# Performance work log

Measured on AMD Instinct MI355X. Metric: run time of the kernel, lower is better.

Reference implementation:

```python
import jax, jax.numpy as jnp
import numpy as np

B, H, W, C = 32, 56, 56, 256
WS = 7            # window size (hard-coded 49=7*7 in original topk modules)
NH = 8            # num heads
HD = C // NH      # head dim = 32
KCH = HD // 2     # channel top-k = 16
KSPT = 28         # spatial top-k
N = WS * WS       # 49 tokens per window
SCALE = HD ** -0.5
MLP_H = 4 * C

def _rel_index(ws):
    coords = np.stack(np.meshgrid(np.arange(ws), np.arange(ws), indexing='ij')).reshape(2, -1)
    rc = (coords[:, :, None] - coords[:, None, :]).transpose(1, 2, 0).astype(np.int64)
    rc[:, :, 0] += ws - 1
    rc[:, :, 1] += ws - 1
    rc[:, :, 0] *= 2 * ws - 1
    return jnp.asarray(rc.sum(-1))  # (N, N)

REL_IDX = _rel_index(WS)

def setup_inputs():
    key = jax.random.key(0)
    ks = jax.random.split(key, 10)
    p = lambda k, shp: jax.random.normal(k, shp, jnp.float32) * 0.02
    return dict(
        x=jax.random.normal(ks[0], (B, H * W, C), jnp.float32),
        norm1_g=jnp.ones((C,), jnp.float32), norm1_b=jnp.zeros((C,), jnp.float32),
        wq=p(ks[1], (C, C)), bq=jnp.zeros((C,), jnp.float32),
        wk=p(ks[2], (C // 2, C // 2)), bk=jnp.zeros((C // 2,), jnp.float32),
        wv=p(ks[3], (C, C)), bv=jnp.zeros((C,), jnp.float32),
        wproj=p(ks[4], (C, C)), bproj=jnp.zeros((C,), jnp.float32),
        wch=p(ks[5], (2 * HD, HD)), bch=jnp.zeros((HD,), jnp.float32),
        rpb_table=p(ks[6], ((2 * WS - 1) ** 2, NH)),
        norm2_g=jnp.ones((C,), jnp.float32), norm2_b=jnp.zeros((C,), jnp.float32),
        w1=p(ks[7], (C, MLP_H)), b1=jnp.zeros((MLP_H,), jnp.float32),
        w2=p(ks[8], (MLP_H, C)), b2=jnp.zeros((C,), jnp.float32),
    )

def _ln(x, g, b):
    mu = x.mean(-1, keepdims=True)
    var = x.var(-1, keepdims=True)
    return (x - mu) / jnp.sqrt(var + 1e-5) * g + b

def reference(x, norm1_g, norm1_b, wq, bq, wk, bk, wv, bv, wproj, bproj,
              wch, bch, rpb_table, norm2_g, norm2_b, w1, b1, w2, b2):
    shortcut = x
    xn = _ln(x, norm1_g, norm1_b).reshape(B, H, W, C)
    # window partition -> (Bw, N, C)
    xw = xn.reshape(B, H // WS, WS, W // WS, WS, C).transpose(0, 1, 3, 2, 4, 5).reshape(-1, N, C)
    Bw = xw.shape[0]
    q = xw @ wq + bq                                                    # (Bw, N, C)
    qh = q.reshape(Bw, N, NH, HD).transpose(0, 2, 1, 3).reshape(Bw * NH, N, HD)
    # ---- channel top-k (ChannelTopk) ----
    feat = jnp.concatenate([qh.mean(1), qh.max(1)], axis=-1)            # (Bn, 2*HD)
    score = jax.nn.softmax(jax.nn.gelu(feat @ wch + bch, approximate=False), axis=1)
    _, cidx = jax.lax.top_k(score, KCH)
    cidx = jnp.sort(cidx, axis=-1)                                      # sorted channel indices
    qcha = jnp.take_along_axis(qh, cidx[:, None, :], axis=2)            # (Bn, N, KCH)
    qcha1 = qcha.reshape(Bw, NH, N, KCH).transpose(0, 2, 1, 3).reshape(Bw, N, C // 2)
    k = qcha1 @ wk + bk                                                 # (Bw, N, C/2)
    # ---- relative position bias ----
    rpb = rpb_table[REL_IDX.reshape(-1)].reshape(N, N, NH).transpose(2, 0, 1)  # (NH, N, N)
    # ---- spatial top-k (SptialTopk) ----
    _, sidx = jax.lax.top_k(qh.mean(-1), KSPT)
    sidx = jnp.sort(sidx, axis=-1)                                      # (Bn, KSPT)
    qal = jnp.take_along_axis(qcha, sidx[:, :, None], axis=1)           # (Bn, KSPT, KCH)
    vsel = jnp.take_along_axis(qh, sidx[:, :, None], axis=1)            # (Bn, KSPT, HD)
    sidx_h = sidx.reshape(Bw, NH, KSPT)
    yal = jnp.take_along_axis(
        jnp.broadcast_to(rpb[None], (Bw, NH, N, N)),
        jnp.broadcast_to(sidx_h[:, :, None, :], (Bw, NH, N, KSPT)), axis=-1)  # (Bw, NH, N, KSPT)
    # ---- attention ----
    v = vsel.reshape(Bw, NH, KSPT, HD).transpose(0, 2, 1, 3).reshape(Bw, KSPT, C)
    v = (v @ wv + bv).reshape(Bw, KSPT, NH, HD).transpose(0, 2, 1, 3)   # (Bw, NH, KSPT, HD)
    qspt = (qal * SCALE).reshape(Bw, NH, KSPT, KCH)
    kh = k.reshape(Bw, N, NH, KCH).transpose(0, 2, 1, 3)                # (Bw, NH, N, KCH)
    attn = jnp.einsum('bnqc,bnkc->bnqk', kh, qspt) + yal                # (Bw, NH, N, KSPT)
    gate = jax.nn.sigmoid(attn.mean(-1))                                # (Bw, NH, N)
    attn = jax.nn.softmax(attn, axis=-1)
    o = jnp.einsum('bnqk,bnkd->bnqd', attn, v) * gate[..., None]        # (Bw, NH, N, HD)
    o = o.transpose(0, 2, 1, 3).reshape(Bw, N, C)
    o = o @ wproj + bproj
    # window reverse -> (B, L, C)
    xr = o.reshape(B, H // WS, W // WS, WS, WS, C).transpose(0, 1, 3, 2, 4, 5).reshape(B, H * W, C)
    x = shortcut + xr
    h = jax.nn.gelu(_ln(x, norm2_g, norm2_b) @ w1 + b1, approximate=False)
    return x + h @ w2 + b2
```

## Files before the change

kernel.cpp:

```cpp
#include <hip/hip_runtime.h>
#include <hip/hip_bf16.h>
#include <cmath>

#define CC 256
#define WSZ 7
#define WWD_ 56
#define NHD 8
#define HDIM 32
#define KCHN 16
#define KSP 28
#define NTOK 49
#define NWIN 2048
#define NBH 16384
#define LL 3136
#define MTOK 100352
#define MLPH 1024
#define SCALE_Q 0.17677669529663689f

typedef float floatx4 __attribute__((ext_vector_type(4)));
typedef __bf16 bf16x8_t __attribute__((ext_vector_type(8)));

__device__ __forceinline__ float gelu_f(float x) {
    return 0.5f * x * (1.0f + erff(x * 0.7071067811865475f));
}

__device__ __forceinline__ void lds_dma16(const void* g, void* l) {
    __builtin_amdgcn_global_load_lds((__attribute__((address_space(1))) void*)(void*)g,
                                     (__attribute__((address_space(3))) void*)l, 16, 0, 0);
}

__global__ __launch_bounds__(64) void ln_stats_k(const float* __restrict__ x,
                                                 float* __restrict__ mu,
                                                 float* __restrict__ rs) {
    int row = blockIdx.x;
    int lane = threadIdx.x;
    float4 v = reinterpret_cast<const float4*>(x + (size_t)row * CC)[lane];
    float s = v.x + v.y + v.z + v.w;
    float s2 = v.x * v.x + v.y * v.y + v.z * v.z + v.w * v.w;
#pragma unroll
    for (int off = 32; off > 0; off >>= 1) {
        s += __shfl_down(s, off);
        s2 += __shfl_down(s2, off);
    }
    if (lane == 0) {
        float m = s * (1.0f / CC);
        float var = s2 * (1.0f / CC) - m * m;
        mu[row] = m;
        rs[row] = rsqrtf(var + 1e-5f);
    }
}

struct GP {
    const float* W;
    const float* bias;
    float* C;
    int N, K;
    const float* x;
    const float* mu;
    const float* rs;
    const float* g;
    const float* be;
};

__global__ __launch_bounds__(256) void gemm_q_k(GP p) {
    __shared__ __align__(16) float As[16][68];
    __shared__ __align__(16) float Bs[16][256];
    const int bm = blockIdx.x * 64;
    const int t = threadIdx.x;
    const int tx = t & 31;
    const int ty = t >> 5;
    const int w = t >> 6;

    const int ar = t >> 2;
    const int ak = (t & 3) * 4;

    const int r = bm + ar;
    int bwi = r / NTOK, n = r - bwi * NTOK;
    int b = bwi >> 6, rem = bwi & 63;
    int hw = rem >> 3, ww = rem & 7;
    int i0 = n / WSZ, j0 = n - i0 * WSZ;
    size_t grow = (size_t)b * LL + (size_t)(hw * WSZ + i0) * WWD_ + (ww * WSZ + j0);
    const float m = p.mu[grow], rsg = p.rs[grow];
    const float* xrow = p.x + grow * CC;

    float acc[8][8] = {};

    for (int k0 = 0; k0 < CC; k0 += 16) {
        {
            const int kk = k0 + ak;
            float4 xv = *reinterpret_cast<const float4*>(xrow + kk);
            float4 gv = *reinterpret_cast<const float4*>(p.g + kk);
            float4 bv = *reinterpret_cast<const float4*>(p.be + kk);
            As[ak + 0][ar] = (xv.x - m) * rsg * gv.x + bv.x;
            As[ak + 1][ar] = (xv.y - m) * rsg * gv.y + bv.y;
            As[ak + 2][ar] = (xv.z - m) * rsg * gv.z + bv.z;
            As[ak + 3][ar] = (xv.w - m) * rsg * gv.w + bv.w;
        }
#pragma unroll
        for (int j = 0; j < 4; ++j) {
            const int c = j * 256 + t;
            const float* gp = p.W + (size_t)(k0 + (c >> 6)) * CC + (c & 63) * 4;
            lds_dma16(gp, (char*)&Bs[0][0] + j * 4096 + w * 1024);
        }
        __syncthreads();
#pragma unroll
        for (int kk = 0; kk < 16; ++kk) {
            float a[8], bb[8];
            *(float4*)&a[0] = *(const float4*)&As[kk][ty * 8];
            *(float4*)&a[4] = *(const float4*)&As[kk][ty * 8 + 4];
            *(float4*)&bb[0] = *(const float4*)&Bs[kk][tx * 8];
            *(float4*)&bb[4] = *(const float4*)&Bs[kk][tx * 8 + 4];
#pragma unroll
            for (int i = 0; i < 8; ++i)
#pragma unroll
                for (int j = 0; j < 8; ++j) acc[i][j] = fmaf(a[i], bb[j], acc[i][j]);
        }
        __syncthreads();
    }

    float bj[8];
#pragma unroll
    for (int j = 0; j < 8; ++j) bj[j] = p.bias[tx * 8 + j];
#pragma unroll
    for (int i = 0; i < 8; ++i) {
        const int row = bm + ty * 8 + i;
        float* crow = p.C + (size_t)row * CC + tx * 8;
#pragma unroll
        for (int j = 0; j < 8; ++j) crow[j] = acc[i][j] + bj[j];
    }
}

struct MG {
    const __hip_bfloat16* A;
    const __hip_bfloat16* B;
    const float* bias;
    int N, K;
    float* Cf;
    __hip_bfloat16* Cb;
    const float* resid;
    int row0;
};

template <int EPI>
__global__ __launch_bounds__(256) void mgemm_k(MG p) {
    __shared__ __align__(16) __hip_bfloat16 As[128 * 32];
    __shared__ __align__(16) __hip_bfloat16 Bs[128 * 32];
    const int bm = blockIdx.x * 128;
    const int bn = blockIdx.y * 128;
    const int t = threadIdx.x;
    const int lane = t & 63;
    const int w = t >> 6;
    const int wm = (w & 1) * 64;
    const int wn = (w >> 1) * 64;
    const int fr = lane & 15;
    const int fk = (lane >> 4) * 8;

    const int m0 = t >> 2, m1 = (t + 256) >> 2;
    const int kc = (t & 3) * 8;
    const __hip_bfloat16* a0 = p.A + (size_t)(bm + m0) * p.K + kc;
    const __hip_bfloat16* a1 = p.A + (size_t)(bm + m1) * p.K + kc;
    const __hip_bfloat16* b0 = p.B + (size_t)(bn + m0) * p.K + kc;
    const __hip_bfloat16* b1 = p.B + (size_t)(bn + m1) * p.K + kc;

    floatx4 acc[4][4] = {};

    for (int k0 = 0; k0 < p.K; k0 += 32) {
        lds_dma16(a0 + k0, &As[w * 512]);
        lds_dma16(a1 + k0, &As[2048 + w * 512]);
        lds_dma16(b0 + k0, &Bs[w * 512]);
        lds_dma16(b1 + k0, &Bs[2048 + w * 512]);
        __syncthreads();
        bf16x8_t af[4], bf[4];
#pragma unroll
        for (int i = 0; i < 4; ++i)
            af[i] = *(const bf16x8_t*)&As[(wm + i * 16 + fr) * 32 + fk];
#pragma unroll
        for (int j = 0; j < 4; ++j)
            bf[j] = *(const bf16x8_t*)&Bs[(wn + j * 16 + fr) * 32 + fk];
#pragma unroll
        for (int i = 0; i < 4; ++i)
#pragma unroll
            for (int j = 0; j < 4; ++j)
                acc[i][j] = __builtin_amdgcn_mfma_f32_16x16x32_bf16(af[i], bf[j], acc[i][j], 0, 0, 0);
        __syncthreads();
    }

    float bj[4];
#pragma unroll
    for (int j = 0; j < 4; ++j) bj[j] = p.bias[bn + wn + j * 16 + fr];
#pragma unroll
    for (int i = 0; i < 4; ++i) {
#pragma unroll
        for (int r = 0; r < 4; ++r) {
            const int m = bm + wm + i * 16 + (lane >> 4) * 4 + r;
#pragma unroll
            for (int j = 0; j < 4; ++j) {
                const int n = bn + wn + j * 16 + fr;
                float v = acc[i][j][r] + bj[j];
                if constexpr (EPI == 0) {
                    p.Cb[(size_t)m * p.N + n] = __float2bfloat16(v);
                } else if constexpr (EPI == 1) {
                    int bwi = m / NTOK, nn = m - bwi * NTOK;
                    int b = bwi >> 6, rem = bwi & 63;
                    int hw = rem >> 3, wwp = rem & 7;
                    int ii = nn / WSZ, jj = nn - ii * WSZ;
                    size_t oidx = ((size_t)b * LL + (size_t)(hw * WSZ + ii) * WWD_ + (wwp * WSZ + jj)) * CC + n;
                    p.Cf[oidx] = v + p.resid[oidx];
                } else if constexpr (EPI == 2) {
                    p.Cb[(size_t)m * p.N + n] = __float2bfloat16(gelu_f(v));
                } else {
                    size_t gr = (size_t)(m + p.row0);
                    p.Cf[gr * p.N + n] = v + p.resid[gr * p.N + n];
                }
            }
        }
    }
}

__global__ __launch_bounds__(256) void wt_k(const float* __restrict__ W,
                                            __hip_bfloat16* __restrict__ Wt, int K, int N) {
    int g = blockIdx.x * 256 + threadIdx.x;
    if (g >= K * N) return;
    int n = g / K, kk = g - n * K;
    Wt[g] = __float2bfloat16(W[(size_t)kk * N + n]);
}

__global__ __launch_bounds__(64) void topk_k(const float* __restrict__ q,
                                             const float* __restrict__ wch,
                                             const float* __restrict__ bch,
                                             short* __restrict__ cidx,
                                             short* __restrict__ sidx) {
    int bnh = blockIdx.x;
    int bwi = bnh >> 3, h = bnh & 7;
    int lane = threadIdx.x;
    __shared__ float tile[NTOK][HDIM + 1];
    __shared__ float feat[2 * HDIM];
    __shared__ float score[HDIM];
    __shared__ float rowm[NTOK];
    const float* qbase = q + ((size_t)bwi * NTOK) * CC + h * HDIM;
    for (int idx = lane; idx < NTOK * HDIM; idx += 64) {
        int n = idx >> 5, d = idx & 31;
        tile[n][d] = qbase[(size_t)n * CC + d];
    }
    __syncthreads();
    if (lane < HDIM) {
        float s = 0.f, mx = -INFINITY;
        for (int n = 0; n < NTOK; ++n) {
            float v = tile[n][lane];
            s += v;
            mx = fmaxf(mx, v);
        }
        feat[lane] = s * (1.0f / NTOK);
        feat[HDIM + lane] = mx;
    }
    if (lane < NTOK) {
        float s = 0.f;
        for (int d = 0; d < HDIM; ++d) s += tile[lane][d];
        rowm[lane] = s;
    }
    __syncthreads();
    if (lane < HDIM) {
        float s = bch[lane];
        for (int j = 0; j < 2 * HDIM; ++j) s += feat[j] * wch[j * HDIM + lane];
        score[lane] = gelu_f(s);
    }
    __syncthreads();
    {
        bool sel = false;
        if (lane < HDIM) {
            float sv = score[lane];
            int rank = 0;
            for (int j = 0; j < HDIM; ++j) {
                float oj = score[j];
                rank += (oj > sv) || (oj == sv && j < lane);
            }
            sel = rank < KCHN;
        }
        unsigned long long m = __ballot(sel);
        if (sel) {
            int pos = __popcll(m & ((1ull << lane) - 1ull));
            cidx[(size_t)bnh * KCHN + pos] = (short)lane;
        }
    }
    {
        bool sel = false;
        if (lane < NTOK) {
            float sv = rowm[lane];
            int rank = 0;
            for (int j = 0; j < NTOK; ++j) {
                float oj = rowm[j];
                rank += (oj > sv) || (oj == sv && j < lane);
            }
            sel = rank < KSP;
        }
        unsigned long long m = __ballot(sel);
        if (sel) {
            int pos = __popcll(m & ((1ull << lane) - 1ull));
            sidx[(size_t)bnh * KSP + pos] = (short)lane;
        }
    }
}

__global__ __launch_bounds__(256) void gather_ch_k(const float* __restrict__ q,
                                                   const short* __restrict__ cidx,
                                                   __hip_bfloat16* __restrict__ ak) {
    int g = blockIdx.x * 256 + threadIdx.x;
    int r = g >> 7, kk = g & 127;
    int bwi = r / NTOK;
    int hp = kk >> 4, c = kk & 15;
    int ci = cidx[((size_t)(bwi * NHD + hp)) * KCHN + c];
    ak[g] = __float2bfloat16(q[(size_t)r * CC + hp * HDIM + ci]);
}

__global__ __launch_bounds__(256) void gather_sp_k(const float* __restrict__ q,
                                                   const short* __restrict__ sidx,
                                                   __hip_bfloat16* __restrict__ av) {
    int g = blockIdx.x * 256 + threadIdx.x;
    int rr = g >> 8, c = g & 255;
    int bwi = rr / KSP, s = rr - bwi * KSP;
    int tok = sidx[((size_t)(bwi * NHD + (c >> 5))) * KSP + s];
    av[g] = __float2bfloat16(q[((size_t)(bwi * NTOK + tok)) * CC + c]);
}

__global__ __launch_bounds__(64) void attn_k(const float* __restrict__ q,
                                             const __hip_bfloat16* __restrict__ kb,
                                             const __hip_bfloat16* __restrict__ vb,
                                             const short* __restrict__ cidx,
                                             const short* __restrict__ sidx,
                                             const float* __restrict__ rpb,
                                             __hip_bfloat16* __restrict__ ob) {
    int bnh = blockIdx.x;
    int bwi = bnh >> 3, h = bnh & 7;
    int lane = threadIdx.x;
    __shared__ float kh_s[NTOK][KCHN + 1];
    __shared__ float qs_s[KSP][KCHN];
    __shared__ float v_s[KSP][HDIM];
    __shared__ int sidx_s[KSP];
    __shared__ int cidx_s[KCHN];
    if (lane < KSP) sidx_s[lane] = sidx[(size_t)bnh * KSP + lane];
    if (lane < KCHN) cidx_s[lane] = cidx[(size_t)bnh * KCHN + lane];
    for (int idx = lane; idx < NTOK * KCHN; idx += 64) {
        int n = idx >> 4, c = idx & 15;
        kh_s[n][c] = __bfloat162float(kb[((size_t)bwi * NTOK + n) * (NHD * KCHN) + h * KCHN + c]);
    }
    for (int idx = lane; idx < KSP * HDIM; idx += 64) {
        int s = idx >> 5, d = idx & 31;
        v_s[s][d] = __bfloat162float(vb[((size_t)bwi * KSP + s) * CC + h * HDIM + d]);
    }
    __syncthreads();
    for (int idx = lane; idx < KSP * KCHN; idx += 64) {
        int s = idx >> 4, c = idx & 15;
        qs_s[s][c] = q[((size_t)bwi * NTOK + sidx_s[s]) * CC + h * HDIM + cidx_s[c]] * SCALE_Q;
    }
    __syncthreads();
    if (lane < NTOK) {
        int i1 = lane / WSZ, j1 = lane - i1 * WSZ;
        float a[KSP];
        float msum = 0.f;
#pragma unroll
        for (int s = 0; s < KSP; ++s) {
            float dot = 0.f;
#pragma unroll
            for (int c = 0; c < KCHN; ++c) dot += kh_s[lane][c] * qs_s[s][c];
            int m = sidx_s[s];
            int i2 = m / WSZ, j2 = m - i2 * WSZ;
            float bias = rpb[(size_t)((i1 - i2 + 6) * 13 + (j1 - j2 + 6)) * NHD + h];
            a[s] = dot + bias;
            msum += a[s];
        }
        float gate = 1.0f / (1.0f + expf(-msum * (1.0f / KSP)));
        float mx = -INFINITY;
#pragma unroll
        for (int s = 0; s < KSP; ++s) mx = fmaxf(mx, a[s]);
        float sum = 0.f;
#pragma unroll
        for (int s = 0; s < KSP; ++s) {
            a[s] = expf(a[s] - mx);
            sum += a[s];
        }
        float inv = gate / sum;
        __hip_bfloat16* orow = ob + ((size_t)bwi * NTOK + lane) * CC + h * HDIM;
#pragma unroll
        for (int d = 0; d < HDIM; ++d) {
            float od = 0.f;
#pragma unroll
            for (int s = 0; s < KSP; ++s) od += a[s] * v_s[s][d];
            orow[d] = __float2bfloat16(od * inv);
        }
    }
}

__global__ __launch_bounds__(64) void ln2_k(const float* __restrict__ x2,
                                            const float* __restrict__ g,
                                            const float* __restrict__ b,
                                            __hip_bfloat16* __restrict__ a2) {
    int row = blockIdx.x;
    int lane = threadIdx.x;
    float4 v = reinterpret_cast<const float4*>(x2 + (size_t)row * CC)[lane];
    float s = v.x + v.y + v.z + v.w;
    float s2 = v.x * v.x + v.y * v.y + v.z * v.z + v.w * v.w;
#pragma unroll
    for (int off = 1; off < 64; off <<= 1) {
        s += __shfl_xor(s, off);
        s2 += __shfl_xor(s2, off);
    }
    float m = s * (1.0f / CC);
    float rsg = rsqrtf(s2 * (1.0f / CC) - m * m + 1e-5f);
    float4 gv = reinterpret_cast<const float4*>(g)[lane];
    float4 bv = reinterpret_cast<const float4*>(b)[lane];
    __hip_bfloat16* orow = a2 + (size_t)row * CC + lane * 4;
    orow[0] = __float2bfloat16((v.x - m) * rsg * gv.x + bv.x);
    orow[1] = __float2bfloat16((v.y - m) * rsg * gv.y + bv.y);
    orow[2] = __float2bfloat16((v.z - m) * rsg * gv.z + bv.z);
    orow[3] = __float2bfloat16((v.w - m) * rsg * gv.w + bv.w);
}

extern "C" void kernel_launch(void* const* d_in, const int* in_sizes, int n_in,
                              void* d_out, int out_size, void* d_ws, size_t ws_size,
                              hipStream_t stream) {
    const float* x   = (const float*)d_in[0];
    const float* n1g = (const float*)d_in[1];
    const float* n1b = (const float*)d_in[2];
    const float* wq  = (const float*)d_in[3];
    const float* bq  = (const float*)d_in[4];
    const float* wk  = (const float*)d_in[5];
    const float* bk  = (const float*)d_in[6];
    const float* wv  = (const float*)d_in[7];
    const float* bv  = (const float*)d_in[8];
    const float* wpj = (const float*)d_in[9];
    const float* bpj = (const float*)d_in[10];
    const float* wch = (const float*)d_in[11];
    const float* bch = (const float*)d_in[12];
    const float* rpb = (const float*)d_in[13];
    const float* n2g = (const float*)d_in[14];
    const float* n2b = (const float*)d_in[15];
    const float* w1  = (const float*)d_in[16];
    const float* b1  = (const float*)d_in[17];
    const float* w2  = (const float*)d_in[18];
    const float* b2  = (const float*)d_in[19];
    float* out = (float*)d_out;

    char* wsb = (char*)d_ws;
    float* qb            = (float*)wsb;
    __hip_bfloat16* g1   = (__hip_bfloat16*)(wsb + 102760448);
    __hip_bfloat16* g2   = (__hip_bfloat16*)(wsb + 128450560);
    __hip_bfloat16* ob   = g1;
    __hip_bfloat16* kb   = (__hip_bfloat16*)(wsb + 157810688);
    __hip_bfloat16* vb   = (__hip_bfloat16*)(wsb + 183500800);
    float* mu1           = (float*)(wsb + 212860928);
    float* rs1           = mu1 + MTOK;
    short* cidx          = (short*)(wsb + 213663744);
    short* sidx          = (short*)(wsb + 214188032);
    __hip_bfloat16* wkt  = (__hip_bfloat16*)(wsb + 215105536);
    __hip_bfloat16* wvt  = (__hip_bfloat16*)(wsb + 215138304);
    __hip_bfloat16* wpt  = (__hip_bfloat16*)(wsb + 215269376);
    __hip_bfloat16* w1t  = (__hip_bfloat16*)(wsb + 215400448);
    __hip_bfloat16* w2t  = (__hip_bfloat16*)(wsb + 215924736);
    __hip_bfloat16* a2   = (__hip_bfloat16*)qb;
    __hip_bfloat16* hb   = (__hip_bfloat16*)(wsb + 51380224);
    if (ws_size < 216449024ULL) return;

    wt_k<<<(128 * 128 + 255) / 256, 256, 0, stream>>>(wk, wkt, 128, 128);
    wt_k<<<(256 * 256 + 255) / 256, 256, 0, stream>>>(wv, wvt, 256, 256);
    wt_k<<<(256 * 256 + 255) / 256, 256, 0, stream>>>(wpj, wpt, 256, 256);
    wt_k<<<(256 * 1024 + 255) / 256, 256, 0, stream>>>(w1, w1t, 256, 1024);
    wt_k<<<(1024 * 256 + 255) / 256, 256, 0, stream>>>(w2, w2t, 1024, 256);

    ln_stats_k<<<MTOK, 64, 0, stream>>>(x, mu1, rs1);

    GP p{};
    p.W = wq; p.bias = bq; p.C = qb; p.N = CC; p.K = CC;
    p.x = x; p.mu = mu1; p.rs = rs1; p.g = n1g; p.be = n1b;
    gemm_q_k<<<dim3(MTOK / 64), 256, 0, stream>>>(p);

    topk_k<<<NBH, 64, 0, stream>>>(qb, wch, bch, cidx, sidx);

    gather_ch_k<<<MTOK * 128 / 256, 256, 0, stream>>>(qb, cidx, g1);
    MG m{};
    m.A = g1; m.B = wkt; m.bias = bk; m.N = 128; m.K = 128; m.Cb = kb;
    mgemm_k<0><<<dim3(MTOK / 128, 1), 256, 0, stream>>>(m);

    gather_sp_k<<<NWIN * KSP * 256 / 256, 256, 0, stream>>>(qb, sidx, g2);
    m = MG{};
    m.A = g2; m.B = wvt; m.bias = bv; m.N = CC; m.K = CC; m.Cb = vb;
    mgemm_k<0><<<dim3(NWIN * KSP / 128, 2), 256, 0, stream>>>(m);

    attn_k<<<NBH, 64, 0, stream>>>(qb, kb, vb, cidx, sidx, rpb, ob);

    m = MG{};
    m.A = ob; m.B = wpt; m.bias = bpj; m.N = CC; m.K = CC; m.Cf = out; m.resid = x;
    mgemm_k<1><<<dim3(MTOK / 128, 2), 256, 0, stream>>>(m);

    ln2_k<<<MTOK, 64, 0, stream>>>(out, n2g, n2b, a2);

    const int CHUNK = MTOK / 4;
    for (int c = 0; c < 4; ++c) {
        int start = c * CHUNK;
        m = MG{};
        m.A = a2 + (size_t)start * CC; m.B = w1t; m.bias = b1;
        m.N = MLPH; m.K = CC; m.Cb = hb;
        mgemm_k<2><<<dim3(CHUNK / 128, MLPH / 128), 256, 0, stream>>>(m);

        m = MG{};
        m.A = hb; m.B = w2t; m.bias = b2; m.N = CC; m.K = MLPH;
        m.Cf = out; m.resid = out; m.row0 = start;
        mgemm_k<3><<<dim3(CHUNK / 128, CC / 128), 256, 0, stream>>>(m);
    }
}
```

Before: 1.141 ms.

## Double-buffer LDS tiles in fused LN+Q GEMM and split B column mapping

The fp32 LayerNorm+Q projection GEMM now keeps two shared-memory buffers. The next K-slice's global loads and DMA are issued before computing on the current slice, and one barrier per iteration is removed. Each thread's 8 output columns are split into two groups of 4, 128 apart, which changes the LDS read pattern to reduce bank conflicts and allows float4 output stores. This costs double the LDS footprint and more live registers for the prefetched A values.

```diff
diff --git a/kernel.cpp b/kernel.cpp
--- a/kernel.cpp
+++ b/kernel.cpp
@@ -63,8 +63,8 @@
 };
 
 __global__ __launch_bounds__(256) void gemm_q_k(GP p) {
-    __shared__ __align__(16) float As[16][68];
-    __shared__ __align__(16) float Bs[16][256];
+    __shared__ __align__(16) float As[2][16][64];
+    __shared__ __align__(16) float Bs[2][16][256];
     const int bm = blockIdx.x * 64;
     const int t = threadIdx.x;
     const int tx = t & 31;
@@ -81,52 +81,78 @@
     int i0 = n / WSZ, j0 = n - i0 * WSZ;
     size_t grow = (size_t)b * LL + (size_t)(hw * WSZ + i0) * WWD_ + (ww * WSZ + j0);
     const float m = p.mu[grow], rsg = p.rs[grow];
-    const float* xrow = p.x + grow * CC;
+    const float* xrow = p.x + grow * CC + ak;
+    const float* gl = p.g + ak;
+    const float* bl = p.be + ak;
 
     float acc[8][8] = {};
 
-    for (int k0 = 0; k0 < CC; k0 += 16) {
-        {
-            const int kk = k0 + ak;
-            float4 xv = *reinterpret_cast<const float4*>(xrow + kk);
-            float4 gv = *reinterpret_cast<const float4*>(p.g + kk);
-            float4 bv = *reinterpret_cast<const float4*>(p.be + kk);
-            As[ak + 0][ar] = (xv.x - m) * rsg * gv.x + bv.x;
-            As[ak + 1][ar] = (xv.y - m) * rsg * gv.y + bv.y;
-            As[ak + 2][ar] = (xv.z - m) * rsg * gv.z + bv.z;
-            As[ak + 3][ar] = (xv.w - m) * rsg * gv.w + bv.w;
-        }
+    auto dma_B = [&](int buf, int k0) {
 #pragma unroll
         for (int j = 0; j < 4; ++j) {
             const int c = j * 256 + t;
             const float* gp = p.W + (size_t)(k0 + (c >> 6)) * CC + (c & 63) * 4;
-            lds_dma16(gp, (char*)&Bs[0][0] + j * 4096 + w * 1024);
-        }
-        __syncthreads();
+            lds_dma16(gp, (char*)&Bs[buf][0][0] + j * 4096 + w * 1024);
+        }
+    };
+    auto write_A = [&](int buf, float4 xv, float4 gv, float4 bv) {
+        As[buf][ak + 0][ar] = (xv.x - m) * rsg * gv.x + bv.x;
+        As[buf][ak + 1][ar] = (xv.y - m) * rsg * gv.y + bv.y;
+        As[buf][ak + 2][ar] = (xv.z - m) * rsg * gv.z + bv.z;
+        As[buf][ak + 3][ar] = (xv.w - m) * rsg * gv.w + bv.w;
+    };
+
+    {
+        float4 xv = *reinterpret_cast<const float4*>(xrow);
+        float4 gv = *reinterpret_cast<const float4*>(gl);
+        float4 bv = *reinterpret_cast<const float4*>(bl);
+        dma_B(0, 0);
+        write_A(0, xv, gv, bv);
+    }
+    __syncthreads();
+
+#pragma unroll
+    for (int it = 0; it < 16; ++it) {
+        const int cur = it & 1;
+        const int nxt = cur ^ 1;
+        float4 xv, gv, bv;
+        if (it < 15) {
+            const int k0 = (it + 1) * 16;
+            xv = *reinterpret_cast<const float4*>(xrow + k0);
+            gv = *reinterpret_cast<const float4*>(gl + k0);
+            bv = *reinterpret_cast<const float4*>(bl + k0);
+            dma_B(nxt, k0);
+        }
 #pragma unroll
         for (int kk = 0; kk < 16; ++kk) {
             float a[8], bb[8];
-            *(float4*)&a[0] = *(const float4*)&As[kk][ty * 8];
-            *(float4*)&a[4] = *(const float4*)&As[kk][ty * 8 + 4];
-            *(float4*)&bb[0] = *(const float4*)&Bs[kk][tx * 8];
-            *(float4*)&bb[4] = *(const float4*)&Bs[kk][tx * 8 + 4];
+            *(float4*)&a[0] = *(const float4*)&As[cur][kk][ty * 8];
+            *(float4*)&a[4] = *(const float4*)&As[cur][kk][ty * 8 + 4];
+            *(float4*)&bb[0] = *(const float4*)&Bs[cur][kk][tx * 4];
+            *(float4*)&bb[4] = *(const float4*)&Bs[cur][kk][128 + tx * 4];
 #pragma unroll
             for (int i = 0; i < 8; ++i)
 #pragma unroll
                 for (int j = 0; j < 8; ++j) acc[i][j] = fmaf(a[i], bb[j], acc[i][j]);
         }
+        if (it < 15) write_A(nxt, xv, gv, bv);
         __syncthreads();
     }
 
-    float bj[8];
-#pragma unroll
-    for (int j = 0; j < 8; ++j) bj[j] = p.bias[tx * 8 + j];
+    float bj0[4], bj1[4];
+#pragma unroll
+    for (int j = 0; j < 4; ++j) {
+        bj0[j] = p.bias[tx * 4 + j];
+        bj1[j] = p.bias[128 + tx * 4 + j];
+    }
 #pragma unroll
     for (int i = 0; i < 8; ++i) {
         const int row = bm + ty * 8 + i;
-        float* crow = p.C + (size_t)row * CC + tx * 8;
-#pragma unroll
-        for (int j = 0; j < 8; ++j) crow[j] = acc[i][j] + bj[j];
+        float* crow = p.C + (size_t)row * CC;
+        float4 o0 = {acc[i][0] + bj0[0], acc[i][1] + bj0[1], acc[i][2] + bj0[2], acc[i][3] + bj0[3]};
+        float4 o1 = {acc[i][4] + bj1[0], acc[i][5] + bj1[1], acc[i][6] + bj1[2], acc[i][7] + bj1[3]};
+        *reinterpret_cast<float4*>(crow + tx * 4) = o0;
+        *reinterpret_cast<float4*>(crow + 128 + tx * 4) = o1;
     }
 }
 
```

After: 1.138 ms. About the same (-0.2%).

## Double-buffer MFMA GEMM tiles, split Q GEMM over N, halve MLP chunks

Applied to the files above, without the earlier changes.

The bf16 MFMA GEMM now uses two LDS buffers, so the next K-tile is DMA'd while the current one feeds the MFMAs. This drops one barrier per iteration and overlaps load latency with compute. The fp32 LayerNorm+Q GEMM is split into two 128-column blocks per row tile, with fewer accumulators and a launch-bounds occupancy hint, to raise parallelism. The MLP now runs in 2 chunks instead of 4, with the hidden buffer moved to a larger workspace region that reuses dead kb/vb space. The costs are doubled LDS in mgemm, recomputing the LayerNorm of A in both Q column blocks, and larger MLP intermediates.

```diff
diff --git a/kernel.cpp b/kernel.cpp
--- a/kernel.cpp
+++ b/kernel.cpp
@@ -62,10 +62,11 @@
     const float* be;
 };
 
-__global__ __launch_bounds__(256) void gemm_q_k(GP p) {
+__global__ __launch_bounds__(256, 6) void gemm_q_k(GP p) {
     __shared__ __align__(16) float As[16][68];
-    __shared__ __align__(16) float Bs[16][256];
+    __shared__ __align__(16) float Bs[16][128];
     const int bm = blockIdx.x * 64;
+    const int bn = blockIdx.y * 128;
     const int t = threadIdx.x;
     const int tx = t & 31;
     const int ty = t >> 5;
@@ -81,52 +82,51 @@
     int i0 = n / WSZ, j0 = n - i0 * WSZ;
     size_t grow = (size_t)b * LL + (size_t)(hw * WSZ + i0) * WWD_ + (ww * WSZ + j0);
     const float m = p.mu[grow], rsg = p.rs[grow];
-    const float* xrow = p.x + grow * CC;
-
-    float acc[8][8] = {};
+    const float* xrow = p.x + grow * CC + ak;
+    const float* gl = p.g + ak;
+    const float* bl = p.be + ak;
+
+    float acc[8][4] = {};
 
     for (int k0 = 0; k0 < CC; k0 += 16) {
         {
-            const int kk = k0 + ak;
-            float4 xv = *reinterpret_cast<const float4*>(xrow + kk);
-            float4 gv = *reinterpret_cast<const float4*>(p.g + kk);
-            float4 bv = *reinterpret_cast<const float4*>(p.be + kk);
+            float4 xv = *reinterpret_cast<const float4*>(xrow + k0);
+            float4 gv = *reinterpret_cast<const float4*>(gl + k0);
+            float4 bv = *reinterpret_cast<const float4*>(bl + k0);
             As[ak + 0][ar] = (xv.x - m) * rsg * gv.x + bv.x;
             As[ak + 1][ar] = (xv.y - m) * rsg * gv.y + bv.y;
             As[ak + 2][ar] = (xv.z - m) * rsg * gv.z + bv.z;
             As[ak + 3][ar] = (xv.w - m) * rsg * gv.w + bv.w;
         }
 #pragma unroll
-        for (int j = 0; j < 4; ++j) {
+        for (int j = 0; j < 2; ++j) {
             const int c = j * 256 + t;
-            const float* gp = p.W + (size_t)(k0 + (c >> 6)) * CC + (c & 63) * 4;
+            const float* gp = p.W + (size_t)(k0 + (c >> 5)) * CC + bn + (c & 31) * 4;
             lds_dma16(gp, (char*)&Bs[0][0] + j * 4096 + w * 1024);
         }
         __syncthreads();
 #pragma unroll
         for (int kk = 0; kk < 16; ++kk) {
-            float a[8], bb[8];
+            float a[8], bb[4];
             *(float4*)&a[0] = *(const float4*)&As[kk][ty * 8];
             *(float4*)&a[4] = *(const float4*)&As[kk][ty * 8 + 4];
-            *(float4*)&bb[0] = *(const float4*)&Bs[kk][tx * 8];
-            *(float4*)&bb[4] = *(const float4*)&Bs[kk][tx * 8 + 4];
+            *(float4*)&bb[0] = *(const float4*)&Bs[kk][tx * 4];
 #pragma unroll
             for (int i = 0; i < 8; ++i)
 #pragma unroll
-                for (int j = 0; j < 8; ++j) acc[i][j] = fmaf(a[i], bb[j], acc[i][j]);
+                for (int j = 0; j < 4; ++j) acc[i][j] = fmaf(a[i], bb[j], acc[i][j]);
         }
         __syncthreads();
     }
 
-    float bj[8];
-#pragma unroll
-    for (int j = 0; j < 8; ++j) bj[j] = p.bias[tx * 8 + j];
+    float bj[4];
+#pragma unroll
+    for (int j = 0; j < 4; ++j) bj[j] = p.bias[bn + tx * 4 + j];
 #pragma unroll
     for (int i = 0; i < 8; ++i) {
         const int row = bm + ty * 8 + i;
-        float* crow = p.C + (size_t)row * CC + tx * 8;
-#pragma unroll
-        for (int j = 0; j < 8; ++j) crow[j] = acc[i][j] + bj[j];
+        float4 o = {acc[i][0] + bj[0], acc[i][1] + bj[1], acc[i][2] + bj[2], acc[i][3] + bj[3]};
+        *reinterpret_cast<float4*>(p.C + (size_t)row * CC + bn + tx * 4) = o;
     }
 }
 
@@ -143,8 +143,8 @@
 
 template <int EPI>
 __global__ __launch_bounds__(256) void mgemm_k(MG p) {
-    __shared__ __align__(16) __hip_bfloat16 As[128 * 32];
-    __shared__ __align__(16) __hip_bfloat16 Bs[128 * 32];
+    __shared__ __align__(16) __hip_bfloat16 As[2][128 * 32];
+    __shared__ __align__(16) __hip_bfloat16 Bs[2][128 * 32];
     const int bm = blockIdx.x * 128;
     const int bn = blockIdx.y * 128;
     const int t = threadIdx.x;
@@ -162,27 +162,34 @@
     const __hip_bfloat16* b0 = p.B + (size_t)(bn + m0) * p.K + kc;
     const __hip_bfloat16* b1 = p.B + (size_t)(bn + m1) * p.K + kc;
 
+    auto stage = [&](int buf, int k0) {
+        lds_dma16(a0 + k0, &As[buf][w * 512]);
+        lds_dma16(a1 + k0, &As[buf][2048 + w * 512]);
+        lds_dma16(b0 + k0, &Bs[buf][w * 512]);
+        lds_dma16(b1 + k0, &Bs[buf][2048 + w * 512]);
+    };
+
     floatx4 acc[4][4] = {};
 
+    stage(0, 0);
+    __syncthreads();
+    int cur = 0;
     for (int k0 = 0; k0 < p.K; k0 += 32) {
-        lds_dma16(a0 + k0, &As[w * 512]);
-        lds_dma16(a1 + k0, &As[2048 + w * 512]);
-        lds_dma16(b0 + k0, &Bs[w * 512]);
-        lds_dma16(b1 + k0, &Bs[2048 + w * 512]);
-        __syncthreads();
+        if (k0 + 32 < p.K) stage(cur ^ 1, k0 + 32);
         bf16x8_t af[4], bf[4];
 #pragma unroll
         for (int i = 0; i < 4; ++i)
-            af[i] = *(const bf16x8_t*)&As[(wm + i * 16 + fr) * 32 + fk];
+            af[i] = *(const bf16x8_t*)&As[cur][(wm + i * 16 + fr) * 32 + fk];
 #pragma unroll
         for (int j = 0; j < 4; ++j)
-            bf[j] = *(const bf16x8_t*)&Bs[(wn + j * 16 + fr) * 32 + fk];
+            bf[j] = *(const bf16x8_t*)&Bs[cur][(wn + j * 16 + fr) * 32 + fk];
 #pragma unroll
         for (int i = 0; i < 4; ++i)
 #pragma unroll
             for (int j = 0; j < 4; ++j)
                 acc[i][j] = __builtin_amdgcn_mfma_f32_16x16x32_bf16(af[i], bf[j], acc[i][j], 0, 0, 0);
         __syncthreads();
+        cur ^= 1;
     }
 
     float bj[4];
@@ -457,7 +464,7 @@
     __hip_bfloat16* w1t  = (__hip_bfloat16*)(wsb + 215400448);
     __hip_bfloat16* w2t  = (__hip_bfloat16*)(wsb + 215924736);
     __hip_bfloat16* a2   = (__hip_bfloat16*)qb;
-    __hip_bfloat16* hb   = (__hip_bfloat16*)(wsb + 51380224);
+    __hip_bfloat16* hb   = (__hip_bfloat16*)(wsb + 102760448);
     if (ws_size < 216449024ULL) return;
 
     wt_k<<<(128 * 128 + 255) / 256, 256, 0, stream>>>(wk, wkt, 128, 128);
@@ -471,7 +478,7 @@
     GP p{};
     p.W = wq; p.bias = bq; p.C = qb; p.N = CC; p.K = CC;
     p.x = x; p.mu = mu1; p.rs = rs1; p.g = n1g; p.be = n1b;
-    gemm_q_k<<<dim3(MTOK / 64), 256, 0, stream>>>(p);
+    gemm_q_k<<<dim3(MTOK / 64, 2), 256, 0, stream>>>(p);
 
     topk_k<<<NBH, 64, 0, stream>>>(qb, wch, bch, cidx, sidx);
 
@@ -493,8 +500,8 @@
 
     ln2_k<<<MTOK, 64, 0, stream>>>(out, n2g, n2b, a2);
 
-    const int CHUNK = MTOK / 4;
-    for (int c = 0; c < 4; ++c) {
+    const int CHUNK = MTOK / 2;
+    for (int c = 0; c < 2; ++c) {
         int start = c * CHUNK;
         m = MG{};
         m.A = a2 + (size_t)start * CC; m.B = w1t; m.bias = b1;
```

Result: slower. 1.189 ms (+4.2%).
